# Optimization experiments

Hardware: AMD Instinct MI355X
Metric: run time of the kernel (lower is better)

Reference implementation:

```python
import jax, jax.numpy as jnp
import numpy as np


def setup_inputs() -> dict:
    key = jax.random.key(0)
    k1, k2 = jax.random.split(key)
    B, H, W, C = 16, 128, 128, 192
    prv = jax.random.normal(k1, (B, H, W, C), dtype=jnp.float32)
    nxt = jax.random.normal(k2, (B, H, W, C), dtype=jnp.float32)
    return {"prv": prv, "nxt": nxt, "search_range": 4}


def reference(prv, nxt, search_range):
    # prv, nxt: [B, H, W, C] (NHWC). Output: [B, H, W, d*d] with d = 2r+1.
    r = int(search_range)
    d = 2 * r + 1
    # Zero-pad nxt by r on both spatial dims (matches ZeroPadding2D(r)).
    pad_nxt = jnp.pad(nxt, ((0, 0), (r, r), (r, r), (0, 0)))
    costs = []
    # Fixed small loop over d*d displacement offsets (81 for r=4); each
    # iteration is one fused multiply + channel-mean over the full tensor.
    for i0 in range(d):
        for j0 in range(d):
            roi = jax.lax.dynamic_slice(pad_nxt, (0, i0, j0, 0), prv.shape)
            costs.append(jnp.mean(prv * roi, axis=3))  # [B, H, W]
    return jnp.stack(costs, axis=3)  # [B, H, W, d*d], offsets in row-major (i0, j0) order
```

## Files before the change

### kernel.cpp

```cpp
#include <hip/hip_runtime.h>


typedef __attribute__((ext_vector_type(8))) short short8;
typedef __attribute__((ext_vector_type(4))) float float4v;
typedef __attribute__((ext_vector_type(2))) unsigned int uint2v;

#define HH 128
#define WW 128
#define CC 192
#define PSTRIDE 80
#define BUFB (256 * PSTRIDE)
#define GROWP 17
#define GWAVE (144 * GROWP)

static __device__ __forceinline__ unsigned int pk2(float lo, float hi) {
    unsigned int r;
    asm("v_cvt_pk_bf16_f32 %0, %1, %2" : "=v"(r) : "v"(lo), "v"(hi));
    return r;
}

static __device__ __forceinline__ short8 cvt8pk(const float* __restrict__ p) {
    float4v f0 = *reinterpret_cast<const float4v*>(p);
    float4v f1 = *reinterpret_cast<const float4v*>(p + 4);
    union { unsigned int u[4]; short8 s; } r;
    r.u[0] = pk2(f0[0], f0[1]);
    r.u[1] = pk2(f0[2], f0[3]);
    r.u[2] = pk2(f1[0], f1[1]);
    r.u[3] = pk2(f1[2], f1[3]);
    return r.s;
}

__global__ __launch_bounds__(256, 4) void costvol_kernel(
    const float* __restrict__ prv,
    const float* __restrict__ nxt,
    float* __restrict__ out)
{
    const int tid  = threadIdx.x;
    const int lane = tid & 63;
    const int wv   = tid >> 6;
    const int m    = lane & 15;
    const int q    = lane >> 4;
    const int wr   = wv >> 1, wc = wv & 1;

    const int wt = blockIdx.x, ht = blockIdx.y, b = blockIdx.z;
    const int h0 = ht * 8, w0 = wt * 8;

    const float* nxt_b = nxt + (size_t)b * HH * WW * CC;
    const float* prv_b = prv + (size_t)b * HH * WW * CC;

    __shared__ alignas(16) unsigned char smem[2 * BUFB];

    const int u32 = tid >> 3;
    const int j   = tid & 7;
    const int hc  = u32 & 15;
    const int d   = u32 >> 4;
    const int wwg = w0 - 4 + hc;
    const bool okw = (wwg >= 0) && (wwg < WW);
    const int wcl = wwg < 0 ? 0 : (wwg > WW - 1 ? WW - 1 : wwg);

    int stage_off[8];
    unsigned okmask = 0;
#pragma unroll
    for (int i = 0; i < 8; ++i) {
        int hh = h0 - 4 + 2 * i + d;
        bool ok = okw && (hh >= 0) && (hh < HH);
        int hcl = hh < 0 ? 0 : (hh > HH - 1 ? HH - 1 : hh);
        stage_off[i] = (hcl * WW + wcl) * CC + j * 4;
        okmask |= (unsigned)ok << i;
    }
    const int wbase = u32 * PSTRIDE + j * 8;

    int roff[9];
#pragma unroll
    for (int s = 0; s < 9; ++s) {
        int n  = s * 16 + m;
        int nr = n / 12, nc = n - nr * 12;
        int P  = (wr * 4 + nr) * 16 + (wc * 4 + nc);
        roff[s] = P * PSTRIDE + q * 16;
    }

    const int pr = m >> 2, pc = m & 3;
    const float* pbase =
        prv_b + ((size_t)(h0 + wr * 4 + pr) * WW + (w0 + wc * 4 + pc)) * CC + q * 8;
    short8 afrag[6];
#pragma unroll
    for (int kk = 0; kk < 6; ++kk) afrag[kk] = cvt8pk(pbase + kk * 32);

    {
        float4v sv[8];
#pragma unroll
        for (int i = 0; i < 8; ++i)
            sv[i] = *reinterpret_cast<const float4v*>(nxt_b + stage_off[i]);
#pragma unroll
        for (int i = 0; i < 8; ++i) {
            uint2v p;
            p.x = pk2(sv[i][0], sv[i][1]);
            p.y = pk2(sv[i][2], sv[i][3]);
            if (!((okmask >> i) & 1u)) { p.x = 0u; p.y = 0u; }
            *reinterpret_cast<uint2v*>(&smem[i * (32 * PSTRIDE) + wbase]) = p;
        }
    }
    __syncthreads();

    float4v acc[9];
#pragma unroll
    for (int s = 0; s < 9; ++s) acc[s] = (float4v){0.f, 0.f, 0.f, 0.f};

#pragma unroll
    for (int kk = 0; kk < 6; ++kk) {
        float4v sv[8];
        if (kk < 5) {
#pragma unroll
            for (int i = 0; i < 8; ++i)
                sv[i] = *reinterpret_cast<const float4v*>(
                    nxt_b + stage_off[i] + (kk + 1) * 32);
        }
        const int rb = (kk & 1) * BUFB;
        short8 a = afrag[kk];
#pragma unroll
        for (int s = 0; s < 9; ++s) {
            short8 bf = *reinterpret_cast<const short8*>(&smem[rb + roff[s]]);
            acc[s] = __builtin_amdgcn_mfma_f32_16x16x32_bf16(a, bf, acc[s], 0, 0, 0);
        }
        if (kk < 5) {
            const int wb = ((kk + 1) & 1) * BUFB;
#pragma unroll
            for (int i = 0; i < 8; ++i) {
                uint2v p;
                p.x = pk2(sv[i][0], sv[i][1]);
                p.y = pk2(sv[i][2], sv[i][3]);
                if (!((okmask >> i) & 1u)) { p.x = 0u; p.y = 0u; }
                *reinterpret_cast<uint2v*>(&smem[wb + i * (32 * PSTRIDE) + wbase]) = p;
            }
        }
        __syncthreads();
    }

    float* Gf = reinterpret_cast<float*>(smem);
    const int gbase = wv * GWAVE;
#pragma unroll
    for (int s = 0; s < 9; ++s) {
        int col = s * 16 + m;
#pragma unroll
        for (int r = 0; r < 4; ++r)
            Gf[gbase + col * GROWP + q * 4 + r] = acc[s][r];
    }
    __syncthreads();

    const float scale = 1.0f / 192.0f;
#pragma unroll
    for (int t = 0; t < 21; ++t) {
        int f = t * 256 + tid;
        if (f < 5184) {
            int p   = f / 81;
            int k   = f - p * 81;
            int i0  = k / 9, j0 = k - i0 * 9;
            int pr8 = p >> 3, pc8 = p & 7;
            int gw  = ((pr8 >> 2) << 1) | (pc8 >> 2);
            int pi  = ((pr8 & 3) << 2) | (pc8 & 3);
            int col = ((pr8 & 3) + i0) * 12 + ((pc8 & 3) + j0);
            float v = Gf[gw * GWAVE + col * GROWP + pi] * scale;
            out[((size_t)(b * HH + (h0 + pr8)) * WW + (w0 + pc8)) * 81 + k] = v;
        }
    }
}

extern "C" void kernel_launch(void* const* d_in, const int* in_sizes, int n_in,
                              void* d_out, int out_size, void* d_ws, size_t ws_size,
                              hipStream_t stream) {
    const float* prv = (const float*)d_in[0];
    const float* nxt = (const float*)d_in[1];
    float* out = (float*)d_out;
    dim3 grid(WW / 8, HH / 8, 16);
    dim3 block(256);
    hipLaunchKernelGGL(costvol_kernel, grid, block, 0, stream, prv, nxt, out);
}
```

Baseline: 431.4 us.

## Stage nxt tiles via async global-to-LDS loads with swizzled fp32 layout

Loads of the nxt halo tile now go straight from global memory into LDS using global_load_lds, so they no longer pass through registers. Tiles are stored in fp32 with an XOR-swizzled layout, and the bf16 packing moves to after each LDS read. Block IDs are remapped so neighbouring tiles run close together in time and share cache, and out-of-bounds rows are zeroed only in edge blocks. The fp32 staging doubles LDS per block, which lowers launch bounds occupancy from 4 to 2, and each B fragment is now converted again on every read.

```diff
diff --git a/kernel.cpp b/kernel.cpp
--- a/kernel.cpp
+++ b/kernel.cpp
@@ -3,13 +3,11 @@
 
 typedef __attribute__((ext_vector_type(8))) short short8;
 typedef __attribute__((ext_vector_type(4))) float float4v;
-typedef __attribute__((ext_vector_type(2))) unsigned int uint2v;
 
 #define HH 128
 #define WW 128
 #define CC 192
-#define PSTRIDE 80
-#define BUFB (256 * PSTRIDE)
+#define BUFB 32768
 #define GROWP 17
 #define GWAVE (144 * GROWP)
 
@@ -30,7 +28,14 @@
     return r.s;
 }
 
-__global__ __launch_bounds__(256, 4) void costvol_kernel(
+static __device__ __forceinline__ void gll16(const float* g, void* l) {
+    __builtin_amdgcn_global_load_lds(
+        (const __attribute__((address_space(1))) unsigned int*)g,
+        (__attribute__((address_space(3))) unsigned int*)l,
+        16, 0, 0);
+}
+
+__global__ __launch_bounds__(256, 2) void costvol_kernel(
     const float* __restrict__ prv,
     const float* __restrict__ nxt,
     float* __restrict__ out)
@@ -42,7 +47,9 @@
     const int q    = lane >> 4;
     const int wr   = wv >> 1, wc = wv & 1;
 
-    const int wt = blockIdx.x, ht = blockIdx.y, b = blockIdx.z;
+    int bid = blockIdx.x + (blockIdx.y << 4) + (blockIdx.z << 8);
+    bid = (bid & 7) * 512 + (bid >> 3);
+    const int wt = bid & 15, ht = (bid >> 4) & 15, b = bid >> 8;
     const int h0 = ht * 8, w0 = wt * 8;
 
     const float* nxt_b = nxt + (size_t)b * HH * WW * CC;
@@ -51,32 +58,33 @@
     __shared__ alignas(16) unsigned char smem[2 * BUFB];
 
     const int u32 = tid >> 3;
-    const int j   = tid & 7;
-    const int hc  = u32 & 15;
-    const int d   = u32 >> 4;
-    const int wwg = w0 - 4 + hc;
+    const int jg  = tid & 7;
+    const int jsw = jg ^ (u32 & 7);
+    const int hcol = u32 & 15;
+    const int dpar = u32 >> 4;
+    const int wwg = w0 - 4 + hcol;
     const bool okw = (wwg >= 0) && (wwg < WW);
     const int wcl = wwg < 0 ? 0 : (wwg > WW - 1 ? WW - 1 : wwg);
 
-    int stage_off[8];
+    const float* gp[8];
     unsigned okmask = 0;
 #pragma unroll
     for (int i = 0; i < 8; ++i) {
-        int hh = h0 - 4 + 2 * i + d;
+        int hh = h0 - 4 + 2 * i + dpar;
         bool ok = okw && (hh >= 0) && (hh < HH);
         int hcl = hh < 0 ? 0 : (hh > HH - 1 ? HH - 1 : hh);
-        stage_off[i] = (hcl * WW + wcl) * CC + j * 4;
+        gp[i] = nxt_b + ((size_t)(hcl * WW + wcl)) * CC + jsw * 4;
         okmask |= (unsigned)ok << i;
     }
-    const int wbase = u32 * PSTRIDE + j * 8;
+    const bool edge = (wt == 0) | (wt == 15) | (ht == 0) | (ht == 15);
 
-    int roff[9];
+    int roffA[9];
 #pragma unroll
     for (int s = 0; s < 9; ++s) {
         int n  = s * 16 + m;
         int nr = n / 12, nc = n - nr * 12;
         int P  = (wr * 4 + nr) * 16 + (wc * 4 + nc);
-        roff[s] = P * PSTRIDE + q * 16;
+        roffA[s] = (P * 128 + q * 32) ^ ((P & 7) << 4);
     }
 
     const int pr = m >> 2, pc = m & 3;
@@ -86,21 +94,25 @@
 #pragma unroll
     for (int kk = 0; kk < 6; ++kk) afrag[kk] = cvt8pk(pbase + kk * 32);
 
-    {
-        float4v sv[8];
+    unsigned char* ldsw = smem + wv * 1024;
+
+#pragma unroll
+    for (int i = 0; i < 8; ++i) gll16(gp[i],      ldsw + 0 * BUFB + i * 4096);
+#pragma unroll
+    for (int i = 0; i < 8; ++i) gll16(gp[i] + 32, ldsw + 1 * BUFB + i * 4096);
+    __syncthreads();
+    if (edge) {
 #pragma unroll
         for (int i = 0; i < 8; ++i)
-            sv[i] = *reinterpret_cast<const float4v*>(nxt_b + stage_off[i]);
-#pragma unroll
-        for (int i = 0; i < 8; ++i) {
-            uint2v p;
-            p.x = pk2(sv[i][0], sv[i][1]);
-            p.y = pk2(sv[i][2], sv[i][3]);
-            if (!((okmask >> i) & 1u)) { p.x = 0u; p.y = 0u; }
-            *reinterpret_cast<uint2v*>(&smem[i * (32 * PSTRIDE) + wbase]) = p;
-        }
+            if (!((okmask >> i) & 1u))
+                *reinterpret_cast<float4v*>(smem + 0 * BUFB + i * 4096 + u32 * 128 + jg * 16)
+                    = (float4v){0.f, 0.f, 0.f, 0.f};
     }
-    __syncthreads();
+    asm volatile("s_waitcnt lgkmcnt(0)" ::: "memory");
+    __builtin_amdgcn_sched_barrier(0);
+    __builtin_amdgcn_s_barrier();
+    __builtin_amdgcn_sched_barrier(0);
+    asm volatile("" ::: "memory");
 
     float4v acc[9];
 #pragma unroll
@@ -108,32 +120,40 @@
 
 #pragma unroll
     for (int kk = 0; kk < 6; ++kk) {
-        float4v sv[8];
-        if (kk < 5) {
-#pragma unroll
-            for (int i = 0; i < 8; ++i)
-                sv[i] = *reinterpret_cast<const float4v*>(
-                    nxt_b + stage_off[i] + (kk + 1) * 32);
-        }
-        const int rb = (kk & 1) * BUFB;
+        const int rb = kk & 1;
         short8 a = afrag[kk];
 #pragma unroll
         for (int s = 0; s < 9; ++s) {
-            short8 bf = *reinterpret_cast<const short8*>(&smem[rb + roff[s]]);
-            acc[s] = __builtin_amdgcn_mfma_f32_16x16x32_bf16(a, bf, acc[s], 0, 0, 0);
+            float4v f0 = *reinterpret_cast<const float4v*>(smem + rb * BUFB + roffA[s]);
+            float4v f1 = *reinterpret_cast<const float4v*>(smem + rb * BUFB + (roffA[s] ^ 16));
+            union { unsigned int u[4]; short8 s8; } fr;
+            fr.u[0] = pk2(f0[0], f0[1]);
+            fr.u[1] = pk2(f0[2], f0[3]);
+            fr.u[2] = pk2(f1[0], f1[1]);
+            fr.u[3] = pk2(f1[2], f1[3]);
+            acc[s] = __builtin_amdgcn_mfma_f32_16x16x32_bf16(a, fr.s8, acc[s], 0, 0, 0);
+        }
+        __syncthreads();
+        if (kk < 4) {
+#pragma unroll
+            for (int i = 0; i < 8; ++i)
+                gll16(gp[i] + (kk + 2) * 32, ldsw + rb * BUFB + i * 4096);
         }
         if (kk < 5) {
-            const int wb = ((kk + 1) & 1) * BUFB;
+            if (edge) {
+                const int zb = (kk + 1) & 1;
 #pragma unroll
-            for (int i = 0; i < 8; ++i) {
-                uint2v p;
-                p.x = pk2(sv[i][0], sv[i][1]);
-                p.y = pk2(sv[i][2], sv[i][3]);
-                if (!((okmask >> i) & 1u)) { p.x = 0u; p.y = 0u; }
-                *reinterpret_cast<uint2v*>(&smem[wb + i * (32 * PSTRIDE) + wbase]) = p;
+                for (int i = 0; i < 8; ++i)
+                    if (!((okmask >> i) & 1u))
+                        *reinterpret_cast<float4v*>(smem + zb * BUFB + i * 4096 + u32 * 128 + jg * 16)
+                            = (float4v){0.f, 0.f, 0.f, 0.f};
             }
+            asm volatile("s_waitcnt lgkmcnt(0)" ::: "memory");
+            __builtin_amdgcn_sched_barrier(0);
+            __builtin_amdgcn_s_barrier();
+            __builtin_amdgcn_sched_barrier(0);
+            asm volatile("" ::: "memory");
         }
-        __syncthreads();
     }
 
     float* Gf = reinterpret_cast<float*>(smem);
```

Result: no change. 435.7 us (+1.0%).
